# Kernel tuning notes

Measured on AMD Instinct MI355X. Metric: run time of the kernel, lower is better.

## Reference

```python
import jax, jax.numpy as jnp
import numpy as np

WIN, SIGMA = 11, 1.5
C1, C2, EPS = 0.01 ** 2, 0.03 ** 2, 1e-8


def _gauss_window(win=WIN, sigma=SIGMA):
    coords = jnp.arange(win, dtype=jnp.float32) - (win - 1) / 2
    g = jnp.exp(-coords ** 2 / (2 * sigma ** 2))
    g = g / g.sum()
    return (g[:, None] * g[None, :])[None, None, :, :]


def setup_inputs() -> dict:
    key = jax.random.key(0)
    k1, k2 = jax.random.split(key)
    N, C, H, W = 32, 1, 512, 512
    x = jax.random.uniform(k1, (N, C, H, W), dtype=jnp.float32)
    y = jax.random.uniform(k2, (N, C, H, W), dtype=jnp.float32)
    w = _gauss_window()
    return {"x": x, "y": y, "w": w}


def _conv(x, w):
    pad = w.shape[-1] // 2
    return jax.lax.conv_general_dilated(
        x, w, window_strides=(1, 1), padding=[(pad, pad), (pad, pad)],
        dimension_numbers=("NCHW", "OIHW", "NCHW"))


def reference(x, y, w):
    w = w.astype(x.dtype)
    n = x.shape[0]
    # One fused conv over all five planes stacked on the batch dim.
    stacked = jnp.concatenate([x, y, x * x, y * y, x * y], axis=0)
    conv = _conv(stacked, w)
    mu_x, mu_y, ex2, ey2, exy = (conv[i * n:(i + 1) * n] for i in range(5))
    mu_x2, mu_y2, mu_xy = mu_x ** 2, mu_y ** 2, mu_x * mu_y
    sig_x2 = ex2 - mu_x2
    sig_y2 = ey2 - mu_y2
    sig_xy = exy - mu_xy
    num = (2 * mu_xy + C1) * (2 * sig_xy + C2)
    den = (mu_x2 + mu_y2 + C1) * (sig_x2 + sig_y2 + C2)
    return jnp.clip(num / (den + EPS), 0.0, 1.0).mean()
```

## Files before the change

kernel.cpp:

```cpp
#include <hip/hip_runtime.h>


#define IMG_H 512
#define IMG_W 512
#define NIMG  32
#define TW    128
#define RROWS 32
#define ITERS (RROWS + 10)
#define LDSW  (TW + 10)

#define C1F  1.0e-4f
#define C2F  9.0e-4f
#define EPSF 1.0e-8f

__global__ __launch_bounds__(TW) void ssim_kernel(
    const float* __restrict__ xg, const float* __restrict__ yg,
    const float* __restrict__ wg, float* __restrict__ out)
{
    const int t    = threadIdx.x;
    const int band = blockIdx.x;
    const int chnk = blockIdx.y;
    const int img  = blockIdx.z;
    const int c0   = band * TW;
    const int r0   = chnk * RROWS;

    const float* xb = xg + (size_t)img * (IMG_H * IMG_W);
    const float* yb = yg + (size_t)img * (IMG_H * IMG_W);

    __shared__ float2 ssd[2][LDSW];
    __shared__ float wredS[2];

    float rs = 0.f;
    {
        const int lane = t & 63;
        if (lane < 11) {
            #pragma unroll
            for (int j = 0; j < 11; ++j) rs += wg[lane * 11 + j];
        }
    }
    float g[11];
    #pragma unroll
    for (int k = 0; k < 11; ++k) {
        int gi = __shfl(__float_as_int(rs), k, 64);
        g[k] = __int_as_float(__builtin_amdgcn_readfirstlane(gi));
    }

    const int colA = c0 + t;
    const int  b2     = (t < 5) ? t : (TW + t);
    const int  colB   = c0 - 5 + b2;
    const bool hasB   = (t < 10);
    const bool colBok = hasB && ((unsigned)colB < IMG_W);

    float rS[11], rD[11], rS2[11], rD2[11];

    float lxA, lyA, lxB, lyB;
    {
        const int r = r0 - 5;
        const bool rv = ((unsigned)r < IMG_H);
        const float* xr = xb + (size_t)r * IMG_W;
        const float* yr = yb + (size_t)r * IMG_W;
        lxA = rv ? xr[colA] : 0.f;
        lyA = rv ? yr[colA] : 0.f;
        lxB = (rv && colBok) ? xr[colB] : 0.f;
        lyB = (rv && colBok) ? yr[colB] : 0.f;
    }

    float acc = 0.f;

    for (int ii = 0; ii < 44; ii += 11) {
        #pragma unroll
        for (int s = 0; s < 11; ++s) {
            const int i = ii + s;
            if (i < ITERS) {
                const int pb = i & 1;
                ssd[pb][5 + t] = make_float2(lxA + lyA, lxA - lyA);
                if (hasB)
                    ssd[pb][b2] = make_float2(lxB + lyB, lxB - lyB);
                __syncthreads();

                {
                    const int r = r0 - 4 + i;
                    const bool rv = ((unsigned)r < IMG_H);
                    const float* xr = xb + (size_t)r * IMG_W;
                    const float* yr = yb + (size_t)r * IMG_W;
                    lxA = rv ? xr[colA] : 0.f;
                    lyA = rv ? yr[colA] : 0.f;
                    lxB = (rv && colBok) ? xr[colB] : 0.f;
                    lyB = (rv && colBok) ? yr[colB] : 0.f;
                }

                float hS = 0.f, hD = 0.f, hS2 = 0.f, hD2 = 0.f;
                #pragma unroll
                for (int k = 0; k < 11; ++k) {
                    const float2 w = ssd[pb][t + k];
                    hS  = fmaf(g[k], w.x, hS);
                    hD  = fmaf(g[k], w.y, hD);
                    hS2 = fmaf(g[k], w.x * w.x, hS2);
                    hD2 = fmaf(g[k], w.y * w.y, hD2);
                }
                rS[s] = hS; rD[s] = hD; rS2[s] = hS2; rD2[s] = hD2;

                if (i >= 10) {
                    float mS = 0.f, mD = 0.f, mS2 = 0.f, mD2 = 0.f;
                    #pragma unroll
                    for (int j = 0; j < 11; ++j) {
                        const int sl = (s + 1 + j) % 11;
                        mS  = fmaf(g[j], rS[sl],  mS);
                        mD  = fmaf(g[j], rD[sl],  mD);
                        mS2 = fmaf(g[j], rS2[sl], mS2);
                        mD2 = fmaf(g[j], rD2[sl], mD2);
                    }
                    const float t1   = mS * mS, t2 = mD * mD;
                    const float a    = 0.5f  * (t1 + t2);
                    const float muxy = 0.25f * (t1 - t2);
                    const float ep   = 0.5f  * (mS2 + mD2);
                    const float eq   = 0.25f * (mS2 - mD2);
                    const float sxy  = eq - muxy;
                    const float ssum = ep - a;
                    const float num  = fmaf(2.f, muxy, C1F) * fmaf(2.f, sxy, C2F);
                    const float den  = (a + C1F) * (ssum + C2F);
                    float v = num * __builtin_amdgcn_rcpf(den + EPSF);
                    acc += fminf(fmaxf(v, 0.f), 1.f);
                }
            }
        }
    }

    #pragma unroll
    for (int off = 32; off > 0; off >>= 1)
        acc += __shfl_down(acc, off, 64);
    __syncthreads();
    if ((t & 63) == 0) wredS[t >> 6] = acc;
    __syncthreads();
    if (t == 0) {
        const float tot = wredS[0] + wredS[1];
        atomicAdd(out, tot * (1.0f / (float)((size_t)NIMG * IMG_H * IMG_W)));
    }
}

extern "C" void kernel_launch(void* const* d_in, const int* in_sizes, int n_in,
                              void* d_out, int out_size, void* d_ws, size_t ws_size,
                              hipStream_t stream) {
    const float* x = (const float*)d_in[0];
    const float* y = (const float*)d_in[1];
    const float* w = (const float*)d_in[2];
    float* out = (float*)d_out;

    hipMemsetAsync(out, 0, sizeof(float), stream);

    dim3 grid(IMG_W / TW, IMG_H / RROWS, NIMG);
    ssim_kernel<<<grid, dim3(TW), 0, stream>>>(x, y, w, out);
}
```

Measured before the change: 135.6 us.

## Give each wavefront its own column band and drop block barriers

Each 64-lane wavefront now handles an independent 64-column band with its own LDS row buffer, so four waves share a 256-thread block. This removes the per-row __syncthreads and the cross-wave reduction, relying on wavefront lockstep for LDS visibility. The cost is a larger halo fraction per column loaded and twice as many atomic adds, since every wave issues its own.

Measured after the change: 161.0 us. 1.19x slower.

```diff
diff --git a/kernel.cpp b/kernel.cpp
--- a/kernel.cpp
+++ b/kernel.cpp
@@ -4,39 +4,37 @@
 #define IMG_H 512
 #define IMG_W 512
 #define NIMG  32
-#define TW    128
+#define WC    64
 #define RROWS 32
 #define ITERS (RROWS + 10)
-#define LDSW  (TW + 10)
+#define LDSW  80
 
 #define C1F  1.0e-4f
 #define C2F  9.0e-4f
 #define EPSF 1.0e-8f
 
-__global__ __launch_bounds__(TW) void ssim_kernel(
+__global__ __launch_bounds__(256) void ssim_kernel(
     const float* __restrict__ xg, const float* __restrict__ yg,
     const float* __restrict__ wg, float* __restrict__ out)
 {
     const int t    = threadIdx.x;
-    const int band = blockIdx.x;
+    const int w    = t >> 6;
+    const int lane = t & 63;
+    const int band = blockIdx.x * 4 + w;
     const int chnk = blockIdx.y;
     const int img  = blockIdx.z;
-    const int c0   = band * TW;
+    const int c0   = band * WC;
     const int r0   = chnk * RROWS;
 
     const float* xb = xg + (size_t)img * (IMG_H * IMG_W);
     const float* yb = yg + (size_t)img * (IMG_H * IMG_W);
 
-    __shared__ float2 ssd[2][LDSW];
-    __shared__ float wredS[2];
+    __shared__ float2 ssd[4][LDSW];
 
     float rs = 0.f;
-    {
-        const int lane = t & 63;
-        if (lane < 11) {
-            #pragma unroll
-            for (int j = 0; j < 11; ++j) rs += wg[lane * 11 + j];
-        }
+    if (lane < 11) {
+        #pragma unroll
+        for (int j = 0; j < 11; ++j) rs += wg[lane * 11 + j];
     }
     float g[11];
     #pragma unroll
@@ -45,10 +43,10 @@
         g[k] = __int_as_float(__builtin_amdgcn_readfirstlane(gi));
     }
 
-    const int colA = c0 + t;
-    const int  b2     = (t < 5) ? t : (TW + t);
+    const int colA = c0 + lane;
+    const int  b2     = (lane < 5) ? lane : (WC + lane);
     const int  colB   = c0 - 5 + b2;
-    const bool hasB   = (t < 10);
+    const bool hasB   = (lane < 10);
     const bool colBok = hasB && ((unsigned)colB < IMG_W);
 
     float rS[11], rD[11], rS2[11], rD2[11];
@@ -72,11 +70,9 @@
         for (int s = 0; s < 11; ++s) {
             const int i = ii + s;
             if (i < ITERS) {
-                const int pb = i & 1;
-                ssd[pb][5 + t] = make_float2(lxA + lyA, lxA - lyA);
+                ssd[w][5 + lane] = make_float2(lxA + lyA, lxA - lyA);
                 if (hasB)
-                    ssd[pb][b2] = make_float2(lxB + lyB, lxB - lyB);
-                __syncthreads();
+                    ssd[w][b2] = make_float2(lxB + lyB, lxB - lyB);
 
                 {
                     const int r = r0 - 4 + i;
@@ -92,11 +88,11 @@
                 float hS = 0.f, hD = 0.f, hS2 = 0.f, hD2 = 0.f;
                 #pragma unroll
                 for (int k = 0; k < 11; ++k) {
-                    const float2 w = ssd[pb][t + k];
-                    hS  = fmaf(g[k], w.x, hS);
-                    hD  = fmaf(g[k], w.y, hD);
-                    hS2 = fmaf(g[k], w.x * w.x, hS2);
-                    hD2 = fmaf(g[k], w.y * w.y, hD2);
+                    const float2 v = ssd[w][lane + k];
+                    hS  = fmaf(g[k], v.x, hS);
+                    hD  = fmaf(g[k], v.y, hD);
+                    hS2 = fmaf(g[k], v.x * v.x, hS2);
+                    hD2 = fmaf(g[k], v.y * v.y, hD2);
                 }
                 rS[s] = hS; rD[s] = hD; rS2[s] = hS2; rD2[s] = hD2;
 
@@ -129,13 +125,8 @@
     #pragma unroll
     for (int off = 32; off > 0; off >>= 1)
         acc += __shfl_down(acc, off, 64);
-    __syncthreads();
-    if ((t & 63) == 0) wredS[t >> 6] = acc;
-    __syncthreads();
-    if (t == 0) {
-        const float tot = wredS[0] + wredS[1];
-        atomicAdd(out, tot * (1.0f / (float)((size_t)NIMG * IMG_H * IMG_W)));
-    }
+    if (lane == 0)
+        atomicAdd(out, acc * (1.0f / (float)((size_t)NIMG * IMG_H * IMG_W)));
 }
 
 extern "C" void kernel_launch(void* const* d_in, const int* in_sizes, int n_in,
@@ -148,6 +139,6 @@
 
     hipMemsetAsync(out, 0, sizeof(float), stream);
 
-    dim3 grid(IMG_W / TW, IMG_H / RROWS, NIMG);
-    ssim_kernel<<<grid, dim3(TW), 0, stream>>>(x, y, w, out);
+    dim3 grid(IMG_W / (4 * WC), IMG_H / RROWS, NIMG);
+    ssim_kernel<<<grid, dim3(256), 0, stream>>>(x, y, w, out);
 }
```

## Process two columns per thread with full-row blocks and packed FMA

Applied to the files above, without the earlier changes.

Each block now covers a full 512-wide image row band with 256 threads, each thread handling two adjacent columns. This removes the halo columns between bands and their reloads. Loads and LDS accesses are vectorized (float2 global, float4 LDS), and the horizontal and vertical Gaussian passes use packed two-wide FMAs that share LDS reads across both output columns. In exchange the block count drops to 512 and each thread holds about twice as many register arrays, which may lower occupancy.

New measurement: 118.9 us. 1.14x faster.

```diff
diff --git a/kernel.cpp b/kernel.cpp
--- a/kernel.cpp
+++ b/kernel.cpp
@@ -1,42 +1,47 @@
 #include <hip/hip_runtime.h>
 
+
+typedef float v2f __attribute__((ext_vector_type(2)));
+typedef float v4f __attribute__((ext_vector_type(4)));
 
 #define IMG_H 512
 #define IMG_W 512
 #define NIMG  32
-#define TW    128
+#define NT    256
 #define RROWS 32
 #define ITERS (RROWS + 10)
-#define LDSW  (TW + 10)
+#define LDSW  524
 
 #define C1F  1.0e-4f
 #define C2F  9.0e-4f
 #define EPSF 1.0e-8f
 
-__global__ __launch_bounds__(TW) void ssim_kernel(
+static __device__ __forceinline__ v2f pkfma(float s, v2f a, v2f b) {
+    v2f sv = {s, s};
+    return __builtin_elementwise_fma(sv, a, b);
+}
+
+__global__ __launch_bounds__(NT) void ssim_kernel(
     const float* __restrict__ xg, const float* __restrict__ yg,
     const float* __restrict__ wg, float* __restrict__ out)
 {
     const int t    = threadIdx.x;
-    const int band = blockIdx.x;
-    const int chnk = blockIdx.y;
-    const int img  = blockIdx.z;
-    const int c0   = band * TW;
+    const int lane = t & 63;
+    const int chnk = blockIdx.x;
+    const int img  = blockIdx.y;
     const int r0   = chnk * RROWS;
+    const int c0   = 2 * t;
 
     const float* xb = xg + (size_t)img * (IMG_H * IMG_W);
     const float* yb = yg + (size_t)img * (IMG_H * IMG_W);
 
-    __shared__ float2 ssd[2][LDSW];
-    __shared__ float wredS[2];
+    __shared__ alignas(16) v2f ssd[2][LDSW];
+    __shared__ float wredS[4];
 
     float rs = 0.f;
-    {
-        const int lane = t & 63;
-        if (lane < 11) {
-            #pragma unroll
-            for (int j = 0; j < 11; ++j) rs += wg[lane * 11 + j];
-        }
+    if (lane < 11) {
+        #pragma unroll
+        for (int j = 0; j < 11; ++j) rs += wg[lane * 11 + j];
     }
     float g[11];
     #pragma unroll
@@ -45,24 +50,20 @@
         g[k] = __int_as_float(__builtin_amdgcn_readfirstlane(gi));
     }
 
-    const int colA = c0 + t;
-    const int  b2     = (t < 5) ? t : (TW + t);
-    const int  colB   = c0 - 5 + b2;
-    const bool hasB   = (t < 10);
-    const bool colBok = hasB && ((unsigned)colB < IMG_W);
+    const v2f z2 = {0.f, 0.f};
 
-    float rS[11], rD[11], rS2[11], rD2[11];
+    if (t < 5)        { ssd[0][1 + t]   = z2; ssd[1][1 + t]   = z2; }
+    else if (t < 10)  { ssd[0][513 + t] = z2; ssd[1][513 + t] = z2; }
 
-    float lxA, lyA, lxB, lyB;
+    v2f rSD[11][2], rQ[11][2];
+
+    v2f pfx, pfy;
     {
         const int r = r0 - 5;
-        const bool rv = ((unsigned)r < IMG_H);
-        const float* xr = xb + (size_t)r * IMG_W;
-        const float* yr = yb + (size_t)r * IMG_W;
-        lxA = rv ? xr[colA] : 0.f;
-        lyA = rv ? yr[colA] : 0.f;
-        lxB = (rv && colBok) ? xr[colB] : 0.f;
-        lyB = (rv && colBok) ? yr[colB] : 0.f;
+        if ((unsigned)r < IMG_H) {
+            pfx = *(const v2f*)(xb + (size_t)r * IMG_W + c0);
+            pfy = *(const v2f*)(yb + (size_t)r * IMG_W + c0);
+        } else { pfx = z2; pfy = z2; }
     }
 
     float acc = 0.f;
@@ -73,54 +74,82 @@
             const int i = ii + s;
             if (i < ITERS) {
                 const int pb = i & 1;
-                ssd[pb][5 + t] = make_float2(lxA + lyA, lxA - lyA);
-                if (hasB)
-                    ssd[pb][b2] = make_float2(lxB + lyB, lxB - lyB);
+                {
+                    const v2f sv = pfx + pfy;
+                    const v2f dv = pfx - pfy;
+                    v4f st = {sv.x, dv.x, sv.y, dv.y};
+                    *(v4f*)&ssd[pb][6 + c0] = st;
+                }
                 __syncthreads();
 
                 {
                     const int r = r0 - 4 + i;
-                    const bool rv = ((unsigned)r < IMG_H);
-                    const float* xr = xb + (size_t)r * IMG_W;
-                    const float* yr = yb + (size_t)r * IMG_W;
-                    lxA = rv ? xr[colA] : 0.f;
-                    lyA = rv ? yr[colA] : 0.f;
-                    lxB = (rv && colBok) ? xr[colB] : 0.f;
-                    lyB = (rv && colBok) ? yr[colB] : 0.f;
+                    if ((unsigned)r < IMG_H) {
+                        pfx = *(const v2f*)(xb + (size_t)r * IMG_W + c0);
+                        pfy = *(const v2f*)(yb + (size_t)r * IMG_W + c0);
+                    } else { pfx = z2; pfy = z2; }
                 }
 
-                float hS = 0.f, hD = 0.f, hS2 = 0.f, hD2 = 0.f;
+                v2f hA = z2, hB = z2, qA = z2, qB = z2;
                 #pragma unroll
-                for (int k = 0; k < 11; ++k) {
-                    const float2 w = ssd[pb][t + k];
-                    hS  = fmaf(g[k], w.x, hS);
-                    hD  = fmaf(g[k], w.y, hD);
-                    hS2 = fmaf(g[k], w.x * w.x, hS2);
-                    hD2 = fmaf(g[k], w.y * w.y, hD2);
+                for (int m = 0; m < 7; ++m) {
+                    const v4f w4 = *(const v4f*)&ssd[pb][c0 + 2 * m];
+                    const v2f e0 = {w4.x, w4.y};
+                    const v2f e1 = {w4.z, w4.w};
+                    {
+                        const int j = 2 * m;
+                        if (j >= 1) {
+                            const v2f f0 = e0 * e0;
+                            if (j <= 11) {
+                                hA = pkfma(g[j - 1], e0, hA);
+                                qA = pkfma(g[j - 1], f0, qA);
+                            }
+                            if (j >= 2) {
+                                hB = pkfma(g[j - 2], e0, hB);
+                                qB = pkfma(g[j - 2], f0, qB);
+                            }
+                        }
+                    }
+                    {
+                        const int j = 2 * m + 1;
+                        if (j <= 12) {
+                            const v2f f1 = e1 * e1;
+                            if (j <= 11) {
+                                hA = pkfma(g[j - 1], e1, hA);
+                                qA = pkfma(g[j - 1], f1, qA);
+                            }
+                            if (j >= 2) {
+                                hB = pkfma(g[j - 2], e1, hB);
+                                qB = pkfma(g[j - 2], f1, qB);
+                            }
+                        }
+                    }
                 }
-                rS[s] = hS; rD[s] = hD; rS2[s] = hS2; rD2[s] = hD2;
+                rSD[s][0] = hA; rSD[s][1] = hB;
+                rQ[s][0]  = qA; rQ[s][1]  = qB;
 
                 if (i >= 10) {
-                    float mS = 0.f, mD = 0.f, mS2 = 0.f, mD2 = 0.f;
                     #pragma unroll
-                    for (int j = 0; j < 11; ++j) {
-                        const int sl = (s + 1 + j) % 11;
-                        mS  = fmaf(g[j], rS[sl],  mS);
-                        mD  = fmaf(g[j], rD[sl],  mD);
-                        mS2 = fmaf(g[j], rS2[sl], mS2);
-                        mD2 = fmaf(g[j], rD2[sl], mD2);
+                    for (int c = 0; c < 2; ++c) {
+                        v2f mSD = z2, mQ = z2;
+                        #pragma unroll
+                        for (int j = 0; j < 11; ++j) {
+                            const int sl = (s + 1 + j) % 11;
+                            mSD = pkfma(g[j], rSD[sl][c], mSD);
+                            mQ  = pkfma(g[j], rQ[sl][c],  mQ);
+                        }
+                        const v2f t2 = mSD * mSD;
+                        const float a    = 0.5f  * (t2.x + t2.y);
+                        const float muxy = 0.25f * (t2.x - t2.y);
+                        const float ep   = 0.5f  * (mQ.x + mQ.y);
+                        const float eq   = 0.25f * (mQ.x - mQ.y);
+                        const float sxy  = eq - muxy;
+                        const float ssum = ep - a;
+                        const float num  = fmaf(2.f, muxy, C1F) * fmaf(2.f, sxy, C2F);
+                        const float den  = (a + C1F) * (ssum + C2F);
+                        float v = num * __builtin_amdgcn_rcpf(den + EPSF);
+                        acc += fminf(fmaxf(v, 0.f), 1.f);
                     }
-                    const float t1   = mS * mS, t2 = mD * mD;
-                    const float a    = 0.5f  * (t1 + t2);
-                    const float muxy = 0.25f * (t1 - t2);
-                    const float ep   = 0.5f  * (mS2 + mD2);
-                    const float eq   = 0.25f * (mS2 - mD2);
-                    const float sxy  = eq - muxy;
-                    const float ssum = ep - a;
-                    const float num  = fmaf(2.f, muxy, C1F) * fmaf(2.f, sxy, C2F);
-                    const float den  = (a + C1F) * (ssum + C2F);
-                    float v = num * __builtin_amdgcn_rcpf(den + EPSF);
-                    acc += fminf(fmaxf(v, 0.f), 1.f);
                 }
             }
         }
@@ -130,10 +159,10 @@
     for (int off = 32; off > 0; off >>= 1)
         acc += __shfl_down(acc, off, 64);
     __syncthreads();
-    if ((t & 63) == 0) wredS[t >> 6] = acc;
+    if (lane == 0) wredS[t >> 6] = acc;
     __syncthreads();
     if (t == 0) {
-        const float tot = wredS[0] + wredS[1];
+        const float tot = (wredS[0] + wredS[1]) + (wredS[2] + wredS[3]);
         atomicAdd(out, tot * (1.0f / (float)((size_t)NIMG * IMG_H * IMG_W)));
     }
 }
@@ -148,6 +177,6 @@
 
     hipMemsetAsync(out, 0, sizeof(float), stream);
 
-    dim3 grid(IMG_W / TW, IMG_H / RROWS, NIMG);
-    ssim_kernel<<<grid, dim3(TW), 0, stream>>>(x, y, w, out);
+    dim3 grid(IMG_H / RROWS, NIMG);
+    ssim_kernel<<<grid, dim3(NT), 0, stream>>>(x, y, w, out);
 }
```
